# Kernel tuning notes

Hardware: AMD Instinct MI355X
Metric: run time of the kernel (lower is better)

Reference implementation:

```python
import jax
jax.config.update("jax_enable_x64", True)
import jax.numpy as jnp
import numpy as np

B = 32768
H = 19
MAX_FLOOD = min(H * H // 4, 100)  # 90, as in the torch module
MAX_HISTORY = 100


def _count_neighbors(m):
    # orthogonal neighbor sum, float [B,H,W] -> [B,H,W]; mirrors shift-based _count_neighbors
    p = jnp.pad(m, ((0, 0), (1, 1), (1, 1)))
    return p[:, :-2, 1:-1] + p[:, 2:, 1:-1] + p[:, 1:-1, :-2] + p[:, 1:-1, 2:]


def _dilate4(m):
    # orthogonal bool dilation on [B,2,H,W]
    p = jnp.pad(m, ((0, 0), (0, 0), (1, 1), (1, 1)))
    return p[:, :, :-2, 1:-1] | p[:, :, 2:, 1:-1] | p[:, :, 1:-1, :-2] | p[:, :, 1:-1, 2:]


def _xor_reduce(x):
    # xor-reduce int64 over last axis (zobrist hash accumulation)
    return jax.lax.reduce(x, np.int64(0), jax.lax.bitwise_xor, (x.ndim - 1,))


def setup_inputs() -> dict:
    key = jax.random.key(0)
    k1, k2, k3, k4, k5 = jax.random.split(key, 5)
    board = jax.random.uniform(k1, (B, H, H), dtype=jnp.float32)
    zobrist_stones = jax.random.randint(k2, (2, H * H), 0, np.int64(2) ** 62, dtype=jnp.int64)
    zobrist_turn = jax.random.randint(k3, (2,), 0, np.int64(2) ** 62, dtype=jnp.int64)
    current_player = jax.random.randint(k4, (B,), 0, 2, dtype=jnp.int32)
    position_history = jax.random.randint(k5, (B, MAX_HISTORY), 0, np.int64(2) ** 62, dtype=jnp.int64)
    return {
        "board": board,
        "zobrist_stones": zobrist_stones,
        "zobrist_turn": zobrist_turn,
        "current_player": current_player,
        "position_history": position_history,
    }


def reference(board, zobrist_stones, zobrist_turn, current_player, position_history):
    black = board > 0.65
    white = board < 0.35
    stones = jnp.stack([black, white], axis=1)            # [B,2,H,W] bool
    empty = (~(black | white)).astype(board.dtype)        # [B,H,W]

    # liberty counts per stone (neighbor counting, as in _count_neighbors)
    nb_empty = _count_neighbors(empty)                    # [B,H,W] float
    lib = nb_empty[:, None] * stones.astype(board.dtype)  # [B,2,H,W]

    # iterative flood fill: grow 'alive' (has-liberty) groups within same color
    seed = stones & (nb_empty[:, None] > 0)
    alive = jax.lax.fori_loop(
        0, MAX_FLOOD, lambda i, a: a | (_dilate4(a) & stones), seed
    )

    # zobrist position hash: XOR of per-point stone hashes + turn hash
    z = zobrist_stones.reshape(2, H, H)
    zero = np.int64(0)
    hb = _xor_reduce(jnp.where(black, z[0], zero).reshape(B, -1))
    hw = _xor_reduce(jnp.where(white, z[1], zero).reshape(B, -1))
    hashes = hb ^ hw ^ zobrist_turn[current_player]       # [B] int64

    # super-ko: does current hash appear anywhere in position history?
    superko = (hashes[:, None] == position_history).any(axis=1)  # [B] bool

    out = jnp.concatenate([lib, alive.astype(board.dtype)], axis=1)  # [B,4,H,W]
    return out, hashes, superko
```

## Files before the change

kernel.cpp:

```cpp
#include <hip/hip_runtime.h>
#include <cstdint>

static constexpr int NBOARD = 32768;
static constexpr int NC = 361;
static constexpr unsigned R19 = 0x7FFFFu;
static constexpr long long C0 = 47316992LL;

__device__ __forceinline__ unsigned long long pick6(int w,
    unsigned long long a0, unsigned long long a1, unsigned long long a2,
    unsigned long long a3, unsigned long long a4, unsigned long long a5)
{
    unsigned long long r = 0ull;
    r = (w == 0) ? a0 : r;
    r = (w == 1) ? a1 : r;
    r = (w == 2) ? a2 : r;
    r = (w == 3) ? a3 : r;
    r = (w == 4) ? a4 : r;
    r = (w == 5) ? a5 : r;
    return r;
}

__global__ __launch_bounds__(256) void go_board_kernel(
    const float* __restrict__ board,
    const unsigned* __restrict__ zst,
    const unsigned* __restrict__ zturn,
    const int* __restrict__ cur,
    const unsigned* __restrict__ hist,
    float* __restrict__ out)
{
    const int lane = threadIdx.x & 63;
    const int b    = (int)((blockIdx.x * blockDim.x + threadIdx.x) >> 6);

    const float* bd = board + (size_t)b * NC;

    unsigned long long bb[6], wb[6];
    unsigned h = 0u;
    #pragma unroll
    for (int c = 0; c < 6; ++c) {
        const int idx = lane + 64 * c;
        const bool valid = (c < 5) || (idx < NC);
        float v = 0.5f;
        unsigned z0 = 0u, z1 = 0u;
        if (valid) {
            v  = bd[idx];
            z0 = zst[idx];
            z1 = zst[NC + idx];
        }
        const bool blk = valid && (v > 0.65f);
        const bool wht = valid && (v < 0.35f);
        bb[c] = __ballot(blk);
        wb[c] = __ballot(wht);
        if (blk) h ^= z0;
        if (wht) h ^= z1;
    }

    #pragma unroll
    for (int off = 32; off >= 1; off >>= 1) h ^= __shfl_xor(h, off);

    const int r = lane & 31;
    const bool isrow = (r < 19);
    const int colw = lane >> 5;

    unsigned long long s0 = colw ? wb[0] : bb[0];
    unsigned long long s1 = colw ? wb[1] : bb[1];
    unsigned long long s2 = colw ? wb[2] : bb[2];
    unsigned long long s3 = colw ? wb[3] : bb[3];
    unsigned long long s4 = colw ? wb[4] : bb[4];
    unsigned long long s5 = colw ? wb[5] : bb[5];

    const int start = 19 * r;
    const int w0 = start >> 6;
    const int sh = start & 63;
    unsigned long long lo64 = pick6(w0,     s0, s1, s2, s3, s4, s5);
    unsigned long long hi64 = pick6(w0 + 1, s0, s1, s2, s3, s4, s5);
    unsigned long long merged = sh ? ((lo64 >> sh) | (hi64 << (64 - sh))) : lo64;
    unsigned stone = isrow ? ((unsigned)merged & R19) : 0u;

    unsigned other = __shfl(stone, lane ^ 32);
    unsigned empt  = isrow ? ((~(stone | other)) & R19) : 0u;

    unsigned eu = __shfl(empt, lane - 1); eu = (r == 0)  ? 0u : eu;
    unsigned ed = __shfl(empt, lane + 1); ed = (r == 18) ? 0u : ed;
    unsigned dil0 = ((empt << 1) | (empt >> 1) | eu | ed);
    unsigned a = stone & dil0;

    #pragma unroll 1
    for (int it = 0; it < 90; ++it) {
        unsigned au = __shfl(a, lane - 1); au = (r == 0)  ? 0u : au;
        unsigned ad = __shfl(a, lane + 1); ad = (r == 18) ? 0u : ad;
        unsigned na = a | (((a << 1) | (a >> 1) | au | ad) & stone);
        const bool ch = (na != a);
        a = na;
        if (!__any(ch)) break;
    }

    const size_t obase = (size_t)b * 1444;

    #pragma unroll
    for (int ch = 0; ch < 2; ++ch) {
        #pragma unroll
        for (int j = 0; j < 6; ++j) {
            const int k  = lane + 64 * j;
            const int kk = (k < NC) ? k : 0;
            const int rr = kk / 19;
            const int cc = kk - rr * 19;
            const int src = (ch << 5) + rr;
            unsigned srow = __shfl(stone, src);
            unsigned e0   = __shfl(empt, src);
            unsigned euu  = __shfl(empt, src - 1);
            unsigned edd  = __shfl(empt, src + 1);
            int cnt = (int)(((e0 << 1) >> cc) & 1u)
                    + (int)((e0 >> (cc + 1)) & 1u)
                    + (rr > 0  ? (int)((euu >> cc) & 1u) : 0)
                    + (rr < 18 ? (int)((edd >> cc) & 1u) : 0);
            int val = ((srow >> cc) & 1u) ? cnt : 0;
            if (k < NC) out[obase + (size_t)(ch * 361 + k)] = (float)val;
        }
    }

    #pragma unroll
    for (int ch = 0; ch < 2; ++ch) {
        #pragma unroll
        for (int j = 0; j < 6; ++j) {
            const int k  = lane + 64 * j;
            const int kk = (k < NC) ? k : 0;
            const int rr = kk / 19;
            const int cc = kk - rr * 19;
            unsigned arow = __shfl(a, (ch << 5) + rr);
            if (k < NC) out[obase + (size_t)((2 + ch) * 361 + k)] = (float)((arow >> cc) & 1u);
        }
    }

    const int cp = cur[b];
    const unsigned hfin = h ^ zturn[cp];

    const unsigned* hb = hist + (size_t)b * 100;
    bool m = (hb[lane] == hfin);
    if (lane < 36) m = m || (hb[64 + lane] == hfin);
    const unsigned long long mb = __ballot(m);

    if (lane == 0) {
        out[C0 + b]          = (float)(int)hfin;
        out[C0 + NBOARD + b] = (mb != 0ull) ? 1.0f : 0.0f;
    }
}

extern "C" void kernel_launch(void* const* d_in, const int* in_sizes, int n_in,
                              void* d_out, int out_size, void* d_ws, size_t ws_size,
                              hipStream_t stream) {
    const float* board     = (const float*)d_in[0];
    const unsigned* zst    = (const unsigned*)d_in[1];
    const unsigned* zturn  = (const unsigned*)d_in[2];
    const int* cur         = (const int*)d_in[3];
    const unsigned* hist   = (const unsigned*)d_in[4];
    float* out = (float*)d_out;

    dim3 grid(NBOARD / 4), block(256);
    hipLaunchKernelGGL(go_board_kernel, grid, block, 0, stream,
                       board, zst, zturn, cur, hist, out);
}
```

Before: 45.35 us.

## Use nontemporal IO, unroll flood fill by two, merge output loops, vectorize history

Board loads, history loads and all output stores now use nontemporal hints, and the history check reads 16-byte vectors across 25 lanes. The flood-fill loop does two dilation steps per convergence vote, and the row-boundary selects are removed because out-of-range lanes hold zero rows. The four output channels are written in one fused loop that shares row-index math and shuffles. The aim is less cache pollution from the large streaming output and fewer instructions per iteration. The cost is up to one extra dilation step after convergence.

Measured after the change: 77.72 us. +71.4%, slower.

```diff
diff --git a/kernel.cpp b/kernel.cpp
--- a/kernel.cpp
+++ b/kernel.cpp
@@ -5,6 +5,8 @@
 static constexpr int NC = 361;
 static constexpr unsigned R19 = 0x7FFFFu;
 static constexpr long long C0 = 47316992LL;
+
+typedef unsigned u32x4 __attribute__((ext_vector_type(4)));
 
 __device__ __forceinline__ unsigned long long pick6(int w,
     unsigned long long a0, unsigned long long a1, unsigned long long a2,
@@ -42,7 +44,7 @@
         float v = 0.5f;
         unsigned z0 = 0u, z1 = 0u;
         if (valid) {
-            v  = bd[idx];
+            v  = __builtin_nontemporal_load(&bd[idx]);
             z0 = zst[idx];
             z1 = zst[NC + idx];
         }
@@ -79,64 +81,57 @@
     unsigned other = __shfl(stone, lane ^ 32);
     unsigned empt  = isrow ? ((~(stone | other)) & R19) : 0u;
 
-    unsigned eu = __shfl(empt, lane - 1); eu = (r == 0)  ? 0u : eu;
-    unsigned ed = __shfl(empt, lane + 1); ed = (r == 18) ? 0u : ed;
-    unsigned dil0 = ((empt << 1) | (empt >> 1) | eu | ed);
-    unsigned a = stone & dil0;
+    unsigned eu = __shfl(empt, lane - 1);
+    unsigned ed = __shfl(empt, lane + 1);
+    unsigned a = stone & ((empt << 1) | (empt >> 1) | eu | ed);
 
     #pragma unroll 1
-    for (int it = 0; it < 90; ++it) {
-        unsigned au = __shfl(a, lane - 1); au = (r == 0)  ? 0u : au;
-        unsigned ad = __shfl(a, lane + 1); ad = (r == 18) ? 0u : ad;
-        unsigned na = a | (((a << 1) | (a >> 1) | au | ad) & stone);
-        const bool ch = (na != a);
-        a = na;
-        if (!__any(ch)) break;
+    for (int it = 0; it < 45; ++it) {
+        const unsigned prev = a;
+        unsigned au = __shfl(a, lane - 1);
+        unsigned ad = __shfl(a, lane + 1);
+        a |= ((a << 1) | (a >> 1) | au | ad) & stone;
+        au = __shfl(a, lane - 1);
+        ad = __shfl(a, lane + 1);
+        a |= ((a << 1) | (a >> 1) | au | ad) & stone;
+        if (!__any(a != prev)) break;
     }
 
     const size_t obase = (size_t)b * 1444;
-
     #pragma unroll
-    for (int ch = 0; ch < 2; ++ch) {
-        #pragma unroll
-        for (int j = 0; j < 6; ++j) {
-            const int k  = lane + 64 * j;
-            const int kk = (k < NC) ? k : 0;
-            const int rr = kk / 19;
-            const int cc = kk - rr * 19;
-            const int src = (ch << 5) + rr;
-            unsigned srow = __shfl(stone, src);
-            unsigned e0   = __shfl(empt, src);
-            unsigned euu  = __shfl(empt, src - 1);
-            unsigned edd  = __shfl(empt, src + 1);
-            int cnt = (int)(((e0 << 1) >> cc) & 1u)
-                    + (int)((e0 >> (cc + 1)) & 1u)
-                    + (rr > 0  ? (int)((euu >> cc) & 1u) : 0)
-                    + (rr < 18 ? (int)((edd >> cc) & 1u) : 0);
-            int val = ((srow >> cc) & 1u) ? cnt : 0;
-            if (k < NC) out[obase + (size_t)(ch * 361 + k)] = (float)val;
-        }
-    }
-
-    #pragma unroll
-    for (int ch = 0; ch < 2; ++ch) {
-        #pragma unroll
-        for (int j = 0; j < 6; ++j) {
-            const int k  = lane + 64 * j;
-            const int kk = (k < NC) ? k : 0;
-            const int rr = kk / 19;
-            const int cc = kk - rr * 19;
-            unsigned arow = __shfl(a, (ch << 5) + rr);
-            if (k < NC) out[obase + (size_t)((2 + ch) * 361 + k)] = (float)((arow >> cc) & 1u);
+    for (int j = 0; j < 6; ++j) {
+        const int k  = lane + 64 * j;
+        const int kk = (k < NC) ? k : 0;
+        const int rr = kk / 19;
+        const int cc = kk - rr * 19;
+        const unsigned e0  = __shfl(empt, rr);
+        const unsigned euu = __shfl(empt, rr - 1);
+        const unsigned edd = __shfl(empt, rr + 1);
+        const int cnt = (int)(((e0 << 1) >> cc) & 1u)
+                      + (int)((e0 >> (cc + 1)) & 1u)
+                      + (int)((euu >> cc) & 1u)
+                      + (int)((edd >> cc) & 1u);
+        const unsigned sb = __shfl(stone, rr);
+        const unsigned sw = __shfl(stone, rr + 32);
+        const unsigned ab = __shfl(a, rr);
+        const unsigned aw = __shfl(a, rr + 32);
+        if (k < NC) {
+            __builtin_nontemporal_store(((sb >> cc) & 1u) ? (float)cnt : 0.0f, &out[obase + (size_t)k]);
+            __builtin_nontemporal_store(((sw >> cc) & 1u) ? (float)cnt : 0.0f, &out[obase + (size_t)(361 + k)]);
+            __builtin_nontemporal_store((float)((ab >> cc) & 1u),              &out[obase + (size_t)(722 + k)]);
+            __builtin_nontemporal_store((float)((aw >> cc) & 1u),              &out[obase + (size_t)(1083 + k)]);
         }
     }
 
     const int cp = cur[b];
     const unsigned hfin = h ^ zturn[cp];
 
-    const unsigned* hb = hist + (size_t)b * 100;
-    bool m = (hb[lane] == hfin);
-    if (lane < 36) m = m || (hb[64 + lane] == hfin);
+    const u32x4* hb4 = (const u32x4*)(hist + (size_t)b * 100);
+    bool m = false;
+    if (lane < 25) {
+        const u32x4 hv = __builtin_nontemporal_load(&hb4[lane]);
+        m = (hv.x == hfin) | (hv.y == hfin) | (hv.z == hfin) | (hv.w == hfin);
+    }
     const unsigned long long mb = __ballot(m);
 
     if (lane == 0) {
```
